# Kernel tuning notes

Hardware: AMD Instinct MI355X
Metric: run time of the kernel (lower is better)

Reference implementation:

```python
import jax, jax.numpy as jnp
import numpy as np
import math

N_HEADS = 16
WINDOW_SIZE = 128
DILATION = 4


def _sparse_mask(S, window, dilation):
    # True = allowed to attend. Sliding window of `window` previous tokens
    # plus dilated positions at i - window - dilation - k*dilation (k >= 0).
    i = jnp.arange(S)[:, None]
    j = jnp.arange(S)[None, :]
    win = (j <= i) & (j >= i - window + 1)
    base = i - window - dilation
    dil = (j <= base) & (jnp.mod(base - j, dilation) == 0)
    return win | dil  # (S, S) bool; causal is implied


def setup_inputs() -> dict:
    key = jax.random.key(0)
    k1, k2, k3 = jax.random.split(key, 3)
    B, S, D = 2, 2048, 1024
    x = jax.random.normal(k1, (B, S, D), dtype=jnp.float32)
    qkv = 0.01 * jax.random.normal(k2, (3 * D, D), dtype=jnp.float32)
    wo = 0.01 * jax.random.normal(k3, (D, D), dtype=jnp.float32)
    return {"x": x, "qkv": qkv, "wo": wo}


def reference(x, qkv, wo):
    B, S, D = x.shape
    H = N_HEADS
    dh = D // H
    QKV = x @ qkv.T                       # (B, S, 3D)
    Q, K, V = jnp.split(QKV, 3, axis=-1)  # each (B, S, D)
    q = Q.reshape(B, S, H, dh)
    k = K.reshape(B, S, H, dh)
    v = V.reshape(B, S, H, dh)
    scores = jnp.einsum('bihd,bjhd->bhij', q, k) / math.sqrt(float(dh))
    mask = _sparse_mask(S, WINDOW_SIZE, DILATION)  # (S, S)
    scores = jnp.where(mask[None, None, :, :], scores, jnp.float32(-jnp.inf))
    attn = jax.nn.softmax(scores, axis=-1)         # (B, H, S, S)
    out = jnp.einsum('bhij,bjhd->bihd', attn, v).reshape(B, S, D)
    return out @ wo.T
```

## Files before the change

### kernel.cpp

```cpp
#include <hip/hip_runtime.h>
#include <hip/hip_bf16.h>


typedef short bf16x8 __attribute__((ext_vector_type(8)));
typedef float f32x4 __attribute__((ext_vector_type(4)));
typedef unsigned short us4 __attribute__((ext_vector_type(4)));

__device__ __forceinline__ unsigned short f2bf(float f){
  unsigned u = __float_as_uint(f);
  u += 0x7FFFu + ((u >> 16) & 1u);
  return (unsigned short)(u >> 16);
}
__device__ __forceinline__ float bf2f(unsigned short h){
  return __uint_as_float(((unsigned)h) << 16);
}

__device__ __forceinline__ void gload_lds16(const unsigned short* g, unsigned short* s){
  __builtin_amdgcn_global_load_lds(
    (const __attribute__((address_space(1))) unsigned int*)(uintptr_t)(const void*)g,
    (__attribute__((address_space(3))) unsigned int*)(uintptr_t)(void*)s,
    16, 0, 0);
}

__global__ void cvt_all(const float* __restrict__ x, const float* __restrict__ qkv,
                        const float* __restrict__ wo,
                        unsigned short* __restrict__ Xb, unsigned short* __restrict__ QKVw,
                        unsigned short* __restrict__ Wb){
  int idx = blockIdx.x * 256 + threadIdx.x;
  const float* s; unsigned short* d; int off;
  if (idx < 1048576){ s = x; d = Xb; off = idx; }
  else if (idx < 1835008){ s = qkv; d = QKVw; off = idx - 1048576; }
  else { if (idx >= 2097152) return; s = wo; d = Wb; off = idx - 1835008; }
  float4 v = ((const float4*)s)[off];
  us4 o;
  o[0] = f2bf(v.x); o[1] = f2bf(v.y); o[2] = f2bf(v.z); o[3] = f2bf(v.w);
  ((us4*)d)[off] = o;
}

template<int EPI>
__global__ __launch_bounds__(256)
void gemm_nt(const unsigned short* __restrict__ A, const unsigned short* __restrict__ B,
             float* __restrict__ C,
             unsigned short* __restrict__ Qb, unsigned short* __restrict__ Kb,
             unsigned short* __restrict__ Kd, unsigned short* __restrict__ Vt,
             unsigned short* __restrict__ Vtd){
  constexpr int K = 1024;
  __shared__ __align__(16) unsigned short sMem[(64 + 128) * 64];
  char* sAb = (char*)sMem;
  char* sBb = (char*)sMem + 8192;

  const int tid  = threadIdx.x;
  const int lane = tid & 63;
  const int w    = tid >> 6;
  const int wr = w >> 1, wc = w & 1;
  const int m0 = blockIdx.x * 64;
  const int n0 = blockIdx.y * 128;

  const unsigned short* srcA[2];
  const unsigned short* srcB[4];
  int ldsA[2], ldsB[4];
  #pragma unroll
  for (int q = 0; q < 2; q++){
    int id  = (w * 2 + q) * 1024 + 16 * lane;
    int row = id >> 7;
    int cb  = (id & 127) ^ ((row & 7) << 4);
    srcA[q] = A + (size_t)(m0 + row) * K + (cb >> 1);
    ldsA[q] = (w * 2 + q) * 1024;
  }
  #pragma unroll
  for (int q = 0; q < 4; q++){
    int id  = (w * 4 + q) * 1024 + 16 * lane;
    int row = id >> 7;
    int cb  = (id & 127) ^ ((row & 7) << 4);
    srcB[q] = B + (size_t)(n0 + row) * K + (cb >> 1);
    ldsB[q] = (w * 4 + q) * 1024;
  }

  const int fr = lane & 15;
  const int kg = lane >> 4;
  const int xr = (fr & 7) << 4;
  const int aBase = (wr * 32 + fr) * 128;
  const int bBase = (wc * 64 + fr) * 128;

  f32x4 acc[2][4] = {};

  for (int t = 0; t < K / 64; t++){
    #pragma unroll
    for (int q = 0; q < 2; q++)
      gload_lds16(srcA[q] + t * 64, (unsigned short*)(sAb + ldsA[q]));
    #pragma unroll
    for (int q = 0; q < 4; q++)
      gload_lds16(srcB[q] + t * 64, (unsigned short*)(sBb + ldsB[q]));
    __syncthreads();
    #pragma unroll
    for (int ks = 0; ks < 2; ks++){
      const int cb = (ks * 64 + kg * 16) ^ xr;
      bf16x8 af[2], bfr[4];
      #pragma unroll
      for (int f = 0; f < 2; f++) af[f]  = *(const bf16x8*)(sAb + aBase + f * 2048 + cb);
      #pragma unroll
      for (int f = 0; f < 4; f++) bfr[f] = *(const bf16x8*)(sBb + bBase + f * 2048 + cb);
      #pragma unroll
      for (int fm = 0; fm < 2; fm++)
        #pragma unroll
        for (int fn = 0; fn < 4; fn++)
          acc[fm][fn] = __builtin_amdgcn_mfma_f32_16x16x32_bf16(af[fm], bfr[fn], acc[fm][fn], 0, 0, 0);
    }
    __syncthreads();
  }

  const int crow = wr * 32 + kg * 4;
  const int ccol = wc * 64 + fr;
  if constexpr (EPI == 0){
    #pragma unroll
    for (int fm = 0; fm < 2; fm++)
      #pragma unroll
      for (int fn = 0; fn < 4; fn++)
        #pragma unroll
        for (int i2 = 0; i2 < 4; i2++)
          C[(size_t)(m0 + crow + fm * 16 + i2) * 1024 + n0 + ccol + fn * 16] = acc[fm][fn][i2];
  } else {
    #pragma unroll
    for (int fn = 0; fn < 4; fn++){
      const int nb = n0 + wc * 64 + 16 * fn;
      const int which = nb >> 10;
      const int hh = (nb >> 6) & 15;
      const int d = (nb & 63) + fr;
      #pragma unroll
      for (int fm = 0; fm < 2; fm++)
        #pragma unroll
        for (int i2 = 0; i2 < 4; i2++){
          const int token = m0 + crow + fm * 16 + i2;
          const int btok = token >> 11;
          const int itok = token & 2047;
          const int bhh = btok * 16 + hh;
          const float val = acc[fm][fn][i2];
          if (which == 0){
            Qb[((size_t)bhh * 2048 + itok) * 64 + d] = f2bf(val * 0.125f);
          } else if (which == 1){
            const unsigned short v = f2bf(val);
            Kb[((size_t)bhh * 2048 + itok) * 64 + d] = v;
            Kd[(((size_t)bhh * 4 + (itok & 3)) * 512 + (itok >> 2)) * 64 + d] = v;
          } else {
            const unsigned short v = f2bf(val);
            Vt[((size_t)bhh * 64 + d) * 2048 + itok] = v;
            Vtd[(((size_t)bhh * 4 + (itok & 3)) * 64 + d) * 512 + (itok >> 2)] = v;
          }
        }
    }
  }
}

__global__ __launch_bounds__(64)
void attn_mfma(const unsigned short* __restrict__ Qb,
               const unsigned short* __restrict__ Kb,
               const unsigned short* __restrict__ Kd,
               const unsigned short* __restrict__ Vt,
               const unsigned short* __restrict__ Vtd,
               unsigned short* __restrict__ AttnP){
  const int lane = threadIdx.x;
  const int r15 = lane & 15;
  const int g   = lane >> 4;
  const int c   = blockIdx.x & 3;
  const int gq  = 15 - (blockIdx.x >> 2);
  const int bh  = blockIdx.y;
  const int b   = bh >> 4;
  const int h   = bh & 15;

  __shared__ __align__(16) unsigned short P_lds[32 * 40];
  __shared__ __align__(16) float sc_lds[32];

  const int i_min = c + 128 * gq;

  const unsigned short* Qb_b  = Qb  + (size_t)bh * 2048 * 64;
  const unsigned short* Kb_b  = Kb  + (size_t)bh * 2048 * 64;
  const unsigned short* Vt_b  = Vt  + (size_t)bh * 64 * 2048;
  const unsigned short* Kd_b  = Kd  + ((size_t)bh * 4 + c) * (512 * 64);
  const unsigned short* Vtd_b = Vtd + ((size_t)bh * 4 + c) * (64 * 512);

  bf16x8 qf[2][2];
  #pragma unroll
  for (int fc = 0; fc < 2; fc++){
    const int i = i_min + 4 * (r15 + 16 * fc);
    #pragma unroll
    for (int kc = 0; kc < 2; kc++)
      qf[fc][kc] = *(const bf16x8*)(Qb_b + (size_t)i * 64 + 32 * kc + 8 * g);
  }

  float mrow[2] = {-1e30f, -1e30f};
  float lrow[2] = {0.f, 0.f};
  f32x4 acc[2][4] = {};

  const int jt0 = (i_min > 127) ? ((i_min - 127) >> 5) : 0;
  const int jt1 = (i_min + 124) >> 5;
  const int ntiles = gq + (jt1 - jt0 + 1);

  for (int tt = 0; tt < ntiles; tt++){
    const bool dil = (tt < gq);
    bf16x8 ka[2][2], vb[4];
    int kbase;
    if (dil){
      const int mb0 = 32 * tt;
      kbase = mb0;
      #pragma unroll
      for (int fr2 = 0; fr2 < 2; fr2++){
        const size_t row = (size_t)(mb0 + 16 * fr2 + r15);
        #pragma unroll
        for (int kc = 0; kc < 2; kc++)
          ka[fr2][kc] = *(const bf16x8*)(Kd_b + row * 64 + 32 * kc + 8 * g);
      }
      #pragma unroll
      for (int fd = 0; fd < 4; fd++)
        vb[fd] = *(const bf16x8*)(Vtd_b + (size_t)(r15 + 16 * fd) * 512 + mb0 + 8 * g);
    } else {
      const int j0 = 32 * (jt0 + tt - gq);
      kbase = j0;
      #pragma unroll
      for (int fr2 = 0; fr2 < 2; fr2++){
        const size_t row = (size_t)(j0 + 16 * fr2 + r15);
        #pragma unroll
        for (int kc = 0; kc < 2; kc++)
          ka[fr2][kc] = *(const bf16x8*)(Kb_b + row * 64 + 32 * kc + 8 * g);
      }
      #pragma unroll
      for (int fd = 0; fd < 4; fd++)
        vb[fd] = *(const bf16x8*)(Vt_b + (size_t)(r15 + 16 * fd) * 2048 + j0 + 8 * g);
    }

    f32x4 sf[2][2];
    #pragma unroll
    for (int fr2 = 0; fr2 < 2; fr2++)
      #pragma unroll
      for (int fc = 0; fc < 2; fc++){
        f32x4 z = {0.f, 0.f, 0.f, 0.f};
        z = __builtin_amdgcn_mfma_f32_16x16x32_bf16(ka[fr2][0], qf[fc][0], z, 0, 0, 0);
        z = __builtin_amdgcn_mfma_f32_16x16x32_bf16(ka[fr2][1], qf[fc][1], z, 0, 0, 0);
        sf[fr2][fc] = z;
      }

    const bool needmask = dil ? (tt == gq - 1) : true;
    if (needmask){
      #pragma unroll
      for (int fr2 = 0; fr2 < 2; fr2++)
        #pragma unroll
        for (int rr = 0; rr < 4; rr++){
          const int kl = kbase + 16 * fr2 + 4 * g + rr;
          #pragma unroll
          for (int fc = 0; fc < 2; fc++){
            const int t = r15 + 16 * fc;
            bool ok;
            if (dil) ok = (kl <= 32 * gq + t - 33);
            else { const int i = i_min + 4 * t; ok = (kl <= i) && (kl >= i - 127); }
            if (!ok) sf[fr2][fc][rr] = -1e30f;
          }
        }
    }

    float pp[2][2][4];
    #pragma unroll
    for (int fc = 0; fc < 2; fc++){
      float mx = sf[0][fc][0];
      #pragma unroll
      for (int fr2 = 0; fr2 < 2; fr2++)
        #pragma unroll
        for (int rr = 0; rr < 4; rr++) mx = fmaxf(mx, sf[fr2][fc][rr]);
      mx = fmaxf(mx, __shfl_xor(mx, 16));
      mx = fmaxf(mx, __shfl_xor(mx, 32));
      const float mn = fmaxf(mrow[fc], mx);
      const float kill = (mn > -1e29f) ? 1.f : 0.f;
      const float scf = __expf(mrow[fc] - mn);
      mrow[fc] = mn;
      float rs = 0.f;
      #pragma unroll
      for (int fr2 = 0; fr2 < 2; fr2++)
        #pragma unroll
        for (int rr = 0; rr < 4; rr++){
          const float pv = __expf(sf[fr2][fc][rr] - mn) * kill;
          pp[fr2][fc][rr] = pv;
          rs += pv;
        }
      rs += __shfl_xor(rs, 16);
      rs += __shfl_xor(rs, 32);
      lrow[fc] = lrow[fc] * scf + rs;
      if (g == 0) sc_lds[r15 + 16 * fc] = scf;
    }

    #pragma unroll
    for (int fc = 0; fc < 2; fc++){
      const int q = r15 + 16 * fc;
      #pragma unroll
      for (int fr2 = 0; fr2 < 2; fr2++){
        us4 wv;
        wv[0] = f2bf(pp[fr2][fc][0]); wv[1] = f2bf(pp[fr2][fc][1]);
        wv[2] = f2bf(pp[fr2][fc][2]); wv[3] = f2bf(pp[fr2][fc][3]);
        *(us4*)(&P_lds[q * 40 + 16 * fr2 + 4 * g]) = wv;
      }
    }

    #pragma unroll
    for (int fq = 0; fq < 2; fq++){
      const f32x4 s4 = *(const f32x4*)(&sc_lds[16 * fq + 4 * g]);
      #pragma unroll
      for (int fd = 0; fd < 4; fd++)
        #pragma unroll
        for (int rr = 0; rr < 4; rr++)
          acc[fq][fd][rr] *= s4[rr];
    }

    bf16x8 pa[2];
    #pragma unroll
    for (int fq = 0; fq < 2; fq++)
      pa[fq] = *(const bf16x8*)(&P_lds[(r15 + 16 * fq) * 40 + 8 * g]);
    #pragma unroll
    for (int fq = 0; fq < 2; fq++)
      #pragma unroll
      for (int fd = 0; fd < 4; fd++)
        acc[fq][fd] = __builtin_amdgcn_mfma_f32_16x16x32_bf16(pa[fq], vb[fd], acc[fq][fd], 0, 0, 0);
  }

  if (g == 0){
    sc_lds[r15]      = 1.f / lrow[0];
    sc_lds[r15 + 16] = 1.f / lrow[1];
  }
  #pragma unroll
  for (int fq = 0; fq < 2; fq++){
    const f32x4 li = *(const f32x4*)(&sc_lds[16 * fq + 4 * g]);
    #pragma unroll
    for (int rr = 0; rr < 4; rr++){
      const int t = 16 * fq + 4 * g + rr;
      const int i = i_min + 4 * t;
      unsigned short* rowp = AttnP + ((size_t)(b * 2048 + i)) * 1024 + h * 64 + r15;
      #pragma unroll
      for (int fd = 0; fd < 4; fd++)
        rowp[16 * fd] = f2bf(acc[fq][fd][rr] * li[rr]);
    }
  }
}

extern "C" void kernel_launch(void* const* d_in, const int* in_sizes, int n_in,
                              void* d_out, int out_size, void* d_ws, size_t ws_size,
                              hipStream_t stream){
  const float* x   = (const float*)d_in[0];
  const float* qkv = (const float*)d_in[1];
  const float* wo  = (const float*)d_in[2];
  float* out = (float*)d_out;

  char* ws = (char*)d_ws;
  const size_t MB = 1024 * 1024;
  unsigned short* Xb    = (unsigned short*)(ws + 0 * MB);
  unsigned short* QKVw  = (unsigned short*)(ws + 8 * MB);
  unsigned short* Wb    = (unsigned short*)(ws + 14 * MB);
  unsigned short* Qb    = (unsigned short*)(ws + 16 * MB);
  unsigned short* Kb    = (unsigned short*)(ws + 24 * MB);
  unsigned short* Kd    = (unsigned short*)(ws + 32 * MB);
  unsigned short* Vt    = (unsigned short*)(ws + 40 * MB);
  unsigned short* Vtd   = (unsigned short*)(ws + 48 * MB);
  unsigned short* AttnP = (unsigned short*)(ws + 56 * MB);

  cvt_all<<<dim3(8192), dim3(256), 0, stream>>>(x, qkv, wo, Xb, QKVw, Wb);

  gemm_nt<1><<<dim3(64, 24), dim3(256), 0, stream>>>(
      Xb, QKVw, (float*)nullptr, Qb, Kb, Kd, Vt, Vtd);

  attn_mfma<<<dim3(64, 32), dim3(64), 0, stream>>>(Qb, Kb, Kd, Vt, Vtd, AttnP);

  gemm_nt<0><<<dim3(64, 8), dim3(256), 0, stream>>>(
      AttnP, Wb, out,
      (unsigned short*)nullptr, (unsigned short*)nullptr, (unsigned short*)nullptr,
      (unsigned short*)nullptr, (unsigned short*)nullptr);
}
```

Before: 204.0 us.

## Split GEMM into QKV 128x128 tile kernel and double-buffered output GEMM

The templated GEMM is split into two kernels. The QKV projection now uses 128x128 tiles (a 4x4 fragment grid per wave), which halves the grid and raises data reuse per LDS load. Its V-transpose epilogue also writes four tokens per vector store. The output projection keeps 64x128 tiles but double-buffers the LDS tiles with explicit vmcnt waits, so global loads overlap the MFMA work. The trade-off is higher register and LDS use, fewer blocks for the QKV GEMM, and hand-written waitcnt/barrier sequencing that could be fragile.

Measured after the change: 200.2 us. No clear change (-1.8%).

```diff
diff --git a/kernel.cpp b/kernel.cpp
--- a/kernel.cpp
+++ b/kernel.cpp
@@ -37,17 +37,115 @@
   ((us4*)d)[off] = o;
 }
 
-template<int EPI>
 __global__ __launch_bounds__(256)
-void gemm_nt(const unsigned short* __restrict__ A, const unsigned short* __restrict__ B,
-             float* __restrict__ C,
-             unsigned short* __restrict__ Qb, unsigned short* __restrict__ Kb,
-             unsigned short* __restrict__ Kd, unsigned short* __restrict__ Vt,
-             unsigned short* __restrict__ Vtd){
+void gemm_qkv(const unsigned short* __restrict__ A, const unsigned short* __restrict__ B,
+              unsigned short* __restrict__ Qb, unsigned short* __restrict__ Kb,
+              unsigned short* __restrict__ Kd, unsigned short* __restrict__ Vt,
+              unsigned short* __restrict__ Vtd){
   constexpr int K = 1024;
-  __shared__ __align__(16) unsigned short sMem[(64 + 128) * 64];
+  __shared__ __align__(16) unsigned short sMem[2 * 128 * 64];
   char* sAb = (char*)sMem;
-  char* sBb = (char*)sMem + 8192;
+  char* sBb = (char*)sMem + 16384;
+
+  const int tid  = threadIdx.x;
+  const int lane = tid & 63;
+  const int w    = tid >> 6;
+  const int wr = w >> 1, wc = w & 1;
+  const int m0 = blockIdx.x * 128;
+  const int n0 = blockIdx.y * 128;
+
+  const unsigned short* srcA[4];
+  const unsigned short* srcB[4];
+  int ldsOff[4];
+  #pragma unroll
+  for (int q = 0; q < 4; q++){
+    int id  = (q * 4 + w) * 1024 + 16 * lane;
+    int row = id >> 7;
+    int cb  = (id & 127) ^ ((row & 7) << 4);
+    srcA[q] = A + (size_t)(m0 + row) * K + (cb >> 1);
+    srcB[q] = B + (size_t)(n0 + row) * K + (cb >> 1);
+    ldsOff[q] = (q * 4 + w) * 1024;
+  }
+
+  const int fr = lane & 15;
+  const int kg = lane >> 4;
+  const int xr = (fr & 7) << 4;
+  const int aBase = (wr * 64 + fr) * 128;
+  const int bBase = (wc * 64 + fr) * 128;
+
+  f32x4 acc[4][4] = {};
+
+  for (int t = 0; t < K / 64; t++){
+    #pragma unroll
+    for (int q = 0; q < 4; q++){
+      gload_lds16(srcA[q] + t * 64, (unsigned short*)(sAb + ldsOff[q]));
+      gload_lds16(srcB[q] + t * 64, (unsigned short*)(sBb + ldsOff[q]));
+    }
+    __syncthreads();
+    #pragma unroll
+    for (int ks = 0; ks < 2; ks++){
+      const int cb = (ks * 64 + kg * 16) ^ xr;
+      bf16x8 af[4], bfr[4];
+      #pragma unroll
+      for (int f = 0; f < 4; f++){
+        af[f]  = *(const bf16x8*)(sAb + aBase + f * 2048 + cb);
+        bfr[f] = *(const bf16x8*)(sBb + bBase + f * 2048 + cb);
+      }
+      #pragma unroll
+      for (int fm = 0; fm < 4; fm++)
+        #pragma unroll
+        for (int fn = 0; fn < 4; fn++)
+          acc[fm][fn] = __builtin_amdgcn_mfma_f32_16x16x32_bf16(af[fm], bfr[fn], acc[fm][fn], 0, 0, 0);
+    }
+    __syncthreads();
+  }
+
+  const int crow = wr * 64 + kg * 4;
+  #pragma unroll
+  for (int fn = 0; fn < 4; fn++){
+    const int nb = n0 + wc * 64 + 16 * fn;
+    const int which = nb >> 10;
+    const int hh = (nb >> 6) & 15;
+    const int d = (nb & 63) + fr;
+    #pragma unroll
+    for (int fm = 0; fm < 4; fm++){
+      const int token0 = m0 + crow + fm * 16;
+      const int btok  = token0 >> 11;
+      const int itok0 = token0 & 2047;
+      const int bhh   = btok * 16 + hh;
+      if (which == 0){
+        #pragma unroll
+        for (int i2 = 0; i2 < 4; i2++)
+          Qb[((size_t)bhh * 2048 + itok0 + i2) * 64 + d] = f2bf(acc[fm][fn][i2] * 0.125f);
+      } else if (which == 1){
+        #pragma unroll
+        for (int i2 = 0; i2 < 4; i2++){
+          const int itok = itok0 + i2;
+          const unsigned short v = f2bf(acc[fm][fn][i2]);
+          Kb[((size_t)bhh * 2048 + itok) * 64 + d] = v;
+          Kd[(((size_t)bhh * 4 + (itok & 3)) * 512 + (itok >> 2)) * 64 + d] = v;
+        }
+      } else {
+        us4 pv;
+        #pragma unroll
+        for (int i2 = 0; i2 < 4; i2++) pv[i2] = f2bf(acc[fm][fn][i2]);
+        *(us4*)(Vt + ((size_t)bhh * 64 + d) * 2048 + itok0) = pv;
+        #pragma unroll
+        for (int i2 = 0; i2 < 4; i2++){
+          const int itok = itok0 + i2;
+          Vtd[((size_t)bhh * 4 + (itok & 3)) * 32768 + (size_t)d * 512 + (itok >> 2)] = pv[i2];
+        }
+      }
+    }
+  }
+}
+
+__global__ __launch_bounds__(256)
+void gemm_out(const unsigned short* __restrict__ A, const unsigned short* __restrict__ B,
+              float* __restrict__ C){
+  constexpr int K = 1024;
+  __shared__ __align__(16) unsigned short sMem[2 * (64 + 128) * 64];
+  char* base0 = (char*)sMem;
 
   const int tid  = threadIdx.x;
   const int lane = tid & 63;
@@ -61,19 +159,19 @@
   int ldsA[2], ldsB[4];
   #pragma unroll
   for (int q = 0; q < 2; q++){
-    int id  = (w * 2 + q) * 1024 + 16 * lane;
+    int id  = (q * 4 + w) * 1024 + 16 * lane;
     int row = id >> 7;
     int cb  = (id & 127) ^ ((row & 7) << 4);
     srcA[q] = A + (size_t)(m0 + row) * K + (cb >> 1);
-    ldsA[q] = (w * 2 + q) * 1024;
+    ldsA[q] = (q * 4 + w) * 1024;
   }
   #pragma unroll
   for (int q = 0; q < 4; q++){
-    int id  = (w * 4 + q) * 1024 + 16 * lane;
+    int id  = (q * 4 + w) * 1024 + 16 * lane;
     int row = id >> 7;
     int cb  = (id & 127) ^ ((row & 7) << 4);
     srcB[q] = B + (size_t)(n0 + row) * K + (cb >> 1);
-    ldsB[q] = (w * 4 + q) * 1024;
+    ldsB[q] = (q * 4 + w) * 1024;
   }
 
   const int fr = lane & 15;
@@ -84,71 +182,57 @@
 
   f32x4 acc[2][4] = {};
 
-  for (int t = 0; t < K / 64; t++){
-    #pragma unroll
-    for (int q = 0; q < 2; q++)
-      gload_lds16(srcA[q] + t * 64, (unsigned short*)(sAb + ldsA[q]));
-    #pragma unroll
-    for (int q = 0; q < 4; q++)
-      gload_lds16(srcB[q] + t * 64, (unsigned short*)(sBb + ldsB[q]));
-    __syncthreads();
+  #pragma unroll
+  for (int q = 0; q < 2; q++) gload_lds16(srcA[q], (unsigned short*)(base0 + ldsA[q]));
+  #pragma unroll
+  for (int q = 0; q < 4; q++) gload_lds16(srcB[q], (unsigned short*)(base0 + 8192 + ldsB[q]));
+
+  int cur = 0;
+  for (int t = 0; t < 16; t++){
+    char* bcur = base0 + cur * 24576;
+    if (t < 15){
+      char* bnxt = base0 + (cur ^ 1) * 24576;
+      #pragma unroll
+      for (int q = 0; q < 2; q++) gload_lds16(srcA[q] + (t + 1) * 64, (unsigned short*)(bnxt + ldsA[q]));
+      #pragma unroll
+      for (int q = 0; q < 4; q++) gload_lds16(srcB[q] + (t + 1) * 64, (unsigned short*)(bnxt + 8192 + ldsB[q]));
+      __builtin_amdgcn_sched_barrier(0);
+      asm volatile("s_waitcnt vmcnt(6)");
+    } else {
+      __builtin_amdgcn_sched_barrier(0);
+      asm volatile("s_waitcnt vmcnt(0)");
+    }
+    __builtin_amdgcn_s_barrier();
+    __builtin_amdgcn_sched_barrier(0);
     #pragma unroll
     for (int ks = 0; ks < 2; ks++){
       const int cb = (ks * 64 + kg * 16) ^ xr;
       bf16x8 af[2], bfr[4];
       #pragma unroll
-      for (int f = 0; f < 2; f++) af[f]  = *(const bf16x8*)(sAb + aBase + f * 2048 + cb);
-      #pragma unroll
-      for (int f = 0; f < 4; f++) bfr[f] = *(const bf16x8*)(sBb + bBase + f * 2048 + cb);
+      for (int f = 0; f < 2; f++) af[f]  = *(const bf16x8*)(bcur + aBase + f * 2048 + cb);
+      #pragma unroll
+      for (int f = 0; f < 4; f++) bfr[f] = *(const bf16x8*)(bcur + 8192 + bBase + f * 2048 + cb);
       #pragma unroll
       for (int fm = 0; fm < 2; fm++)
         #pragma unroll
         for (int fn = 0; fn < 4; fn++)
           acc[fm][fn] = __builtin_amdgcn_mfma_f32_16x16x32_bf16(af[fm], bfr[fn], acc[fm][fn], 0, 0, 0);
     }
-    __syncthreads();
+    asm volatile("s_waitcnt lgkmcnt(0)" ::: "memory");
+    __builtin_amdgcn_sched_barrier(0);
+    __builtin_amdgcn_s_barrier();
+    cur ^= 1;
   }
 
   const int crow = wr * 32 + kg * 4;
   const int ccol = wc * 64 + fr;
-  if constexpr (EPI == 0){
-    #pragma unroll
-    for (int fm = 0; fm < 2; fm++)
-      #pragma unroll
-      for (int fn = 0; fn < 4; fn++)
-        #pragma unroll
-        for (int i2 = 0; i2 < 4; i2++)
-          C[(size_t)(m0 + crow + fm * 16 + i2) * 1024 + n0 + ccol + fn * 16] = acc[fm][fn][i2];
-  } else {
-    #pragma unroll
-    for (int fn = 0; fn < 4; fn++){
-      const int nb = n0 + wc * 64 + 16 * fn;
-      const int which = nb >> 10;
-      const int hh = (nb >> 6) & 15;
-      const int d = (nb & 63) + fr;
-      #pragma unroll
-      for (int fm = 0; fm < 2; fm++)
-        #pragma unroll
-        for (int i2 = 0; i2 < 4; i2++){
-          const int token = m0 + crow + fm * 16 + i2;
-          const int btok = token >> 11;
-          const int itok = token & 2047;
-          const int bhh = btok * 16 + hh;
-          const float val = acc[fm][fn][i2];
-          if (which == 0){
-            Qb[((size_t)bhh * 2048 + itok) * 64 + d] = f2bf(val * 0.125f);
-          } else if (which == 1){
-            const unsigned short v = f2bf(val);
-            Kb[((size_t)bhh * 2048 + itok) * 64 + d] = v;
-            Kd[(((size_t)bhh * 4 + (itok & 3)) * 512 + (itok >> 2)) * 64 + d] = v;
-          } else {
-            const unsigned short v = f2bf(val);
-            Vt[((size_t)bhh * 64 + d) * 2048 + itok] = v;
-            Vtd[(((size_t)bhh * 4 + (itok & 3)) * 64 + d) * 512 + (itok >> 2)] = v;
-          }
-        }
-    }
-  }
+  #pragma unroll
+  for (int fm = 0; fm < 2; fm++)
+    #pragma unroll
+    for (int fn = 0; fn < 4; fn++)
+      #pragma unroll
+      for (int i2 = 0; i2 < 4; i2++)
+        C[(size_t)(m0 + crow + fm * 16 + i2) * 1024 + n0 + ccol + fn * 16] = acc[fm][fn][i2];
 }
 
 __global__ __launch_bounds__(64)
@@ -359,13 +443,9 @@
 
   cvt_all<<<dim3(8192), dim3(256), 0, stream>>>(x, qkv, wo, Xb, QKVw, Wb);
 
-  gemm_nt<1><<<dim3(64, 24), dim3(256), 0, stream>>>(
-      Xb, QKVw, (float*)nullptr, Qb, Kb, Kd, Vt, Vtd);
+  gemm_qkv<<<dim3(32, 24), dim3(256), 0, stream>>>(Xb, QKVw, Qb, Kb, Kd, Vt, Vtd);
 
   attn_mfma<<<dim3(64, 32), dim3(64), 0, stream>>>(Qb, Kb, Kd, Vt, Vtd, AttnP);
 
-  gemm_nt<0><<<dim3(64, 8), dim3(256), 0, stream>>>(
-      AttnP, Wb, out,
-      (unsigned short*)nullptr, (unsigned short*)nullptr, (unsigned short*)nullptr,
-      (unsigned short*)nullptr, (unsigned short*)nullptr);
-}
+  gemm_out<<<dim3(64, 8), dim3(256), 0, stream>>>(AttnP, Wb, out);
+}
```
